# Kernel optimization log

Hardware: AMD Instinct MI355X
Metric: run time of the kernel (lower is better)

Reference implementation:

```python
import jax, jax.numpy as jnp
import numpy as np

B, S, E, HD = 32, 1024, 768, 64
NUM_IMAGE_PATCHES = 49


def setup_inputs() -> dict:
    key = jax.random.key(0)
    ks = jax.random.split(key, 9)
    w = 0.02
    return {
        "decoder_sequence": jax.random.normal(ks[0], (B, S, E), dtype=jnp.float32),
        "Wq": jax.random.normal(ks[1], (E, HD), dtype=jnp.float32) * w,
        "bq": jnp.zeros((HD,), dtype=jnp.float32),
        "Wk": jax.random.normal(ks[2], (E, HD), dtype=jnp.float32) * w,
        "bk": jnp.zeros((HD,), dtype=jnp.float32),
        "Wv": jax.random.normal(ks[3], (E, HD), dtype=jnp.float32) * w,
        "bv": jnp.zeros((HD,), dtype=jnp.float32),
        "input_sequence_length": 975,
        "padding_mask": jax.random.randint(ks[4], (B, 1, S), 0, 2).astype(bool),
    }


def reference(decoder_sequence, Wq, bq, Wk, bk, Wv, bv, input_sequence_length, padding_mask):
    # single-head projections: [B,S,E] @ [E,HD] -> [B,S,HD]
    Q = decoder_sequence @ Wq + bq
    K = decoder_sequence @ Wk + bk
    V = decoder_sequence @ Wv + bv

    scores = jnp.einsum('bid,bjd->bij', Q, K) / jnp.sqrt(jnp.float32(HD))

    # mask: image-patch rows (i < 49) fully unmasked; text region is causal
    # (mask[49:,49:] = triu(-inf, diag=1)), i.e. -inf where i >= 49 and j > i.
    i = jnp.arange(S)[:, None]
    j = jnp.arange(S)[None, :]
    causal_bad = (i >= NUM_IMAGE_PATCHES) & (j > i)  # [S,S]
    scores = jnp.where(causal_bad[None, :, :], -jnp.inf, scores)

    # padding mask on keys, broadcast over queries: [B,1,S] -> [B,S,S]
    scores = jnp.where(padding_mask, -jnp.inf, scores)

    A = jax.nn.softmax(scores, axis=-1)
    H = jnp.einsum('bij,bjd->bid', A, V)
    return H
```

## Files before the change

### kernel.cpp

```cpp
#include <hip/hip_runtime.h>
#include <stdint.h>
#include <stddef.h>


typedef __attribute__((ext_vector_type(8))) short bf16x8;
typedef __attribute__((ext_vector_type(4))) float f32x4;

#define NIP 49
#define QSCALE 0.18033688011112042f

__device__ __forceinline__ short f2b(float f) {
  union { float f; uint32_t u; } c; c.f = f;
  uint32_t u = c.u;
  uint32_t r = (u + 0x7fffu + ((u >> 16) & 1u)) >> 16;
  return (short)(uint16_t)r;
}

__global__ __launch_bounds__(256) void wt_kernel(
    const float* __restrict__ Wq, const float* __restrict__ Wk,
    const float* __restrict__ Wv, short* __restrict__ Wt) {
  int idx = blockIdx.x * 256 + threadIdx.x;
  int n = idx % 192;
  int k = idx / 192;
  const float* W = (n < 64) ? Wq : (n < 128) ? Wk : Wv;
  int h = n & 63;
  Wt[(size_t)n * 768 + k] = f2b(W[(size_t)k * 64 + h]);
}

__global__ __launch_bounds__(256) void proj_kernel(
    const float* __restrict__ X, const float* __restrict__ bq,
    const float* __restrict__ bk, const float* __restrict__ bv,
    const short* __restrict__ Wt, short* __restrict__ Qg,
    short* __restrict__ Kg, short* __restrict__ Vg) {
  __shared__ short lX[64][40];
  __shared__ short lW[192][40];
  const int tid = threadIdx.x;
  const int wid = tid >> 6;
  const int lane = tid & 63;
  const int l15 = lane & 15;
  const int q4 = lane >> 4;
  const int r0 = blockIdx.x * 64;

  f32x4 acc[12];
#pragma unroll
  for (int c = 0; c < 12; ++c) acc[c] = (f32x4){0.f, 0.f, 0.f, 0.f};

  for (int k0 = 0; k0 < 768; k0 += 32) {
    __syncthreads();
#pragma unroll
    for (int i = 0; i < 2; ++i) {
      int idx = tid + i * 256;
      int row = idx >> 3, c4 = idx & 7;
      float4 v = *(const float4*)(X + (size_t)(r0 + row) * 768 + k0 + c4 * 4);
      short4 sv;
      sv.x = f2b(v.x); sv.y = f2b(v.y); sv.z = f2b(v.z); sv.w = f2b(v.w);
      *(short4*)&lX[row][c4 * 4] = sv;
    }
#pragma unroll
    for (int i = 0; i < 3; ++i) {
      int idx = tid + i * 256;
      int row = idx >> 2, seg = idx & 3;
      *(int4*)&lW[row][seg * 8] = *(const int4*)(Wt + (size_t)row * 768 + k0 + seg * 8);
    }
    __syncthreads();
    bf16x8 a = *(const bf16x8*)&lX[wid * 16 + l15][q4 * 8];
#pragma unroll
    for (int c = 0; c < 12; ++c) {
      bf16x8 bw = *(const bf16x8*)&lW[c * 16 + l15][q4 * 8];
      acc[c] = __builtin_amdgcn_mfma_f32_16x16x32_bf16(a, bw, acc[c], 0, 0, 0);
    }
  }
#pragma unroll
  for (int c = 0; c < 12; ++c) {
    const int mtx = c >> 2;
    const int h = (c & 3) * 16 + l15;
    const float* bp = (mtx == 0) ? bq : (mtx == 1) ? bk : bv;
    short* op = (mtx == 0) ? Qg : (mtx == 1) ? Kg : Vg;
    const float bias = bp[h];
#pragma unroll
    for (int rr = 0; rr < 4; ++rr) {
      int row = r0 + wid * 16 + q4 * 4 + rr;
      float v = acc[c][rr] + bias;
      if (mtx == 0) v *= QSCALE;
      op[(size_t)row * 64 + h] = f2b(v);
    }
  }
}

__global__ __launch_bounds__(256) void attn_kernel(
    const short* __restrict__ Qg, const short* __restrict__ Kg,
    const short* __restrict__ Vg, const int* __restrict__ pad,
    float* __restrict__ out) {
  __shared__ short lK[64][72];
  __shared__ short lV[64][72];
  __shared__ short lP[4][16][72];
  __shared__ float lpad[64];

  const int t = blockIdx.x, b = blockIdx.y;
  const int tid = threadIdx.x;
  const int wid = tid >> 6;
  const int lane = tid & 63;
  const int l15 = lane & 15;
  const int q4 = lane >> 4;
  const int qs = t * 64;
  const size_t base = (size_t)b * 1024;

  short(*lQ)[72] = (short(*)[72])lP;
#pragma unroll
  for (int i = 0; i < 2; ++i) {
    int idx = tid + i * 256;
    int row = idx >> 3, seg = idx & 7;
    *(int4*)&lQ[row][seg * 8] = *(const int4*)(Qg + (base + qs + row) * 64 + seg * 8);
  }
  __syncthreads();
  bf16x8 aq0 = *(const bf16x8*)&lQ[wid * 16 + l15][q4 * 8];
  bf16x8 aq1 = *(const bf16x8*)&lQ[wid * 16 + l15][32 + q4 * 8];

  f32x4 o[4];
  float m_run[4], l_run[4];
#pragma unroll
  for (int c = 0; c < 4; ++c) o[c] = (f32x4){0.f, 0.f, 0.f, 0.f};
#pragma unroll
  for (int rr = 0; rr < 4; ++rr) { m_run[rr] = -1e30f; l_run[rr] = 0.f; }

  const int nkt = (t == 0) ? 16 : (t + 1);
  for (int kt = 0; kt < nkt; ++kt) {
    const int kb = kt * 64;
    __syncthreads();
#pragma unroll
    for (int i = 0; i < 2; ++i) {
      int idx = tid + i * 256;
      int row = idx >> 3, seg = idx & 7;
      *(int4*)&lK[row][seg * 8] = *(const int4*)(Kg + (base + kb + row) * 64 + seg * 8);
    }
#pragma unroll
    for (int i = 0; i < 2; ++i) {
      int idx = tid + i * 256;
      int row = idx >> 3, seg = idx & 7;
      short tmp[8];
      *(int4*)tmp = *(const int4*)(Vg + (base + kb + row) * 64 + seg * 8);
#pragma unroll
      for (int j = 0; j < 8; ++j) lV[seg * 8 + j][row] = tmp[j];
    }
    if (tid < 64) lpad[tid] = (pad[base + kb + tid] != 0) ? -1e30f : 0.0f;
    __syncthreads();

    f32x4 s[4];
#pragma unroll
    for (int c = 0; c < 4; ++c) {
      s[c] = (f32x4){0.f, 0.f, 0.f, 0.f};
      bf16x8 b0 = *(const bf16x8*)&lK[c * 16 + l15][q4 * 8];
      s[c] = __builtin_amdgcn_mfma_f32_16x16x32_bf16(aq0, b0, s[c], 0, 0, 0);
      bf16x8 b1 = *(const bf16x8*)&lK[c * 16 + l15][32 + q4 * 8];
      s[c] = __builtin_amdgcn_mfma_f32_16x16x32_bf16(aq1, b1, s[c], 0, 0, 0);
    }

    float padv[4];
#pragma unroll
    for (int c = 0; c < 4; ++c) padv[c] = lpad[c * 16 + l15];

    float p[4][4];
#pragma unroll
    for (int rr = 0; rr < 4; ++rr) {
      const int qi = qs + wid * 16 + q4 * 4 + rr;
      float zmax = -1e30f;
#pragma unroll
      for (int c = 0; c < 4; ++c) {
        float z = s[c][rr] + padv[c];
        int j = kb + c * 16 + l15;
        if (qi >= NIP && j > qi) z = -1e30f;
        p[c][rr] = z;
        zmax = fmaxf(zmax, z);
      }
#pragma unroll
      for (int off = 1; off < 16; off <<= 1)
        zmax = fmaxf(zmax, __shfl_xor(zmax, off, 64));
      const float mn = fmaxf(m_run[rr], zmax);
      const float alpha = exp2f(m_run[rr] - mn);
      m_run[rr] = mn;
      float rs = 0.f;
#pragma unroll
      for (int c = 0; c < 4; ++c) {
        float pv = exp2f(p[c][rr] - mn);
        p[c][rr] = pv;
        rs += pv;
      }
#pragma unroll
      for (int off = 1; off < 16; off <<= 1)
        rs += __shfl_xor(rs, off, 64);
      l_run[rr] = l_run[rr] * alpha + rs;
#pragma unroll
      for (int c = 0; c < 4; ++c) o[c][rr] *= alpha;
    }

#pragma unroll
    for (int rr = 0; rr < 4; ++rr)
#pragma unroll
      for (int c = 0; c < 4; ++c)
        lP[wid][q4 * 4 + rr][c * 16 + l15] = f2b(p[c][rr]);
    __syncthreads();

    bf16x8 ap0 = *(const bf16x8*)&lP[wid][l15][q4 * 8];
    bf16x8 ap1 = *(const bf16x8*)&lP[wid][l15][32 + q4 * 8];
#pragma unroll
    for (int c = 0; c < 4; ++c) {
      bf16x8 bv0 = *(const bf16x8*)&lV[c * 16 + l15][q4 * 8];
      o[c] = __builtin_amdgcn_mfma_f32_16x16x32_bf16(ap0, bv0, o[c], 0, 0, 0);
      bf16x8 bv1 = *(const bf16x8*)&lV[c * 16 + l15][32 + q4 * 8];
      o[c] = __builtin_amdgcn_mfma_f32_16x16x32_bf16(ap1, bv1, o[c], 0, 0, 0);
    }
  }

#pragma unroll
  for (int rr = 0; rr < 4; ++rr) {
    const float inv = (l_run[rr] > 0.f) ? 1.0f / l_run[rr] : 0.f;
    const size_t row = base + qs + wid * 16 + q4 * 4 + rr;
#pragma unroll
    for (int c = 0; c < 4; ++c)
      out[row * 64 + c * 16 + l15] = o[c][rr] * inv;
  }
}

extern "C" void kernel_launch(void* const* d_in, const int* in_sizes, int n_in,
                              void* d_out, int out_size, void* d_ws, size_t ws_size,
                              hipStream_t stream) {
  const float* X  = (const float*)d_in[0];
  const float* Wq = (const float*)d_in[1];
  const float* bq = (const float*)d_in[2];
  const float* Wk = (const float*)d_in[3];
  const float* bk = (const float*)d_in[4];
  const float* Wv = (const float*)d_in[5];
  const float* bv = (const float*)d_in[6];
  const int* pad  = (const int*)d_in[8];
  float* out = (float*)d_out;

  short* Qg = (short*)d_ws;
  short* Kg = Qg + 32768 * 64;
  short* Vg = Kg + 32768 * 64;
  short* Wt = Vg + 32768 * 64;

  wt_kernel<<<576, 256, 0, stream>>>(Wq, Wk, Wv, Wt);
  proj_kernel<<<512, 256, 0, stream>>>(X, bq, bk, bv, Wt, Qg, Kg, Vg);
  attn_kernel<<<dim3(16, 32), 256, 0, stream>>>(Qg, Kg, Vg, pad, out);
}
```

Baseline: 237.9 us.

## Double-buffer projection and attention tiles, store V transposed, reorder causal tiles

Measured after the change: 217.8 us. -8.4%, faster.

```diff
diff --git a/kernel.cpp b/kernel.cpp
--- a/kernel.cpp
+++ b/kernel.cpp
@@ -8,6 +8,7 @@
 
 #define NIP 49
 #define QSCALE 0.18033688011112042f
+#define SOFT_BARRIER() asm volatile("s_waitcnt lgkmcnt(0)\n\ts_barrier" ::: "memory")
 
 __device__ __forceinline__ short f2b(float f) {
   union { float f; uint32_t u; } c; c.f = f;
@@ -20,83 +21,107 @@
     const float* __restrict__ Wq, const float* __restrict__ Wk,
     const float* __restrict__ Wv, short* __restrict__ Wt) {
   int idx = blockIdx.x * 256 + threadIdx.x;
-  int n = idx % 192;
-  int k = idx / 192;
+  int n = idx / 768;
+  int k = idx - n * 768;
   const float* W = (n < 64) ? Wq : (n < 128) ? Wk : Wv;
-  int h = n & 63;
-  Wt[(size_t)n * 768 + k] = f2b(W[(size_t)k * 64 + h]);
-}
-
-__global__ __launch_bounds__(256) void proj_kernel(
+  Wt[idx] = f2b(W[(size_t)k * 64 + (n & 63)]);
+}
+
+__global__ __launch_bounds__(512, 4) void proj_kernel(
     const float* __restrict__ X, const float* __restrict__ bq,
     const float* __restrict__ bk, const float* __restrict__ bv,
     const short* __restrict__ Wt, short* __restrict__ Qg,
-    short* __restrict__ Kg, short* __restrict__ Vg) {
-  __shared__ short lX[64][40];
-  __shared__ short lW[192][40];
+    short* __restrict__ Kg, short* __restrict__ Vt) {
+  __shared__ short lX[2][64][40];
+  __shared__ short lW[2][192][40];
   const int tid = threadIdx.x;
   const int wid = tid >> 6;
   const int lane = tid & 63;
   const int l15 = lane & 15;
   const int q4 = lane >> 4;
+  const int mw = wid & 3;
+  const int nh = wid >> 2;
   const int r0 = blockIdx.x * 64;
 
-  f32x4 acc[12];
-#pragma unroll
-  for (int c = 0; c < 12; ++c) acc[c] = (f32x4){0.f, 0.f, 0.f, 0.f};
-
-  for (int k0 = 0; k0 < 768; k0 += 32) {
-    __syncthreads();
-#pragma unroll
-    for (int i = 0; i < 2; ++i) {
-      int idx = tid + i * 256;
-      int row = idx >> 3, c4 = idx & 7;
-      float4 v = *(const float4*)(X + (size_t)(r0 + row) * 768 + k0 + c4 * 4);
+  const int xrow = tid >> 3, xc4 = tid & 7;
+  const int wrow0 = tid >> 2, wseg0 = tid & 3;
+  const int wrow1 = (tid + 512) >> 2, wseg1 = tid & 3;
+
+  float4 rx;
+  int4 rw0, rw1;
+  auto loadg = [&](int k0) {
+    rx = *(const float4*)(X + (size_t)(r0 + xrow) * 768 + k0 + xc4 * 4);
+    rw0 = *(const int4*)(Wt + (size_t)wrow0 * 768 + k0 + wseg0 * 8);
+    if (tid < 256)
+      rw1 = *(const int4*)(Wt + (size_t)wrow1 * 768 + k0 + wseg1 * 8);
+  };
+  auto stage = [&](int buf) {
+    short4 sv;
+    sv.x = f2b(rx.x); sv.y = f2b(rx.y); sv.z = f2b(rx.z); sv.w = f2b(rx.w);
+    *(short4*)&lX[buf][xrow][xc4 * 4] = sv;
+    *(int4*)&lW[buf][wrow0][wseg0 * 8] = rw0;
+    if (tid < 256) *(int4*)&lW[buf][wrow1][wseg1 * 8] = rw1;
+  };
+
+  f32x4 acc[6];
+#pragma unroll
+  for (int c = 0; c < 6; ++c) acc[c] = (f32x4){0.f, 0.f, 0.f, 0.f};
+
+  loadg(0);
+  stage(0);
+  loadg(32);
+  SOFT_BARRIER();
+  for (int st = 0; st < 24; ++st) {
+    const int cur = st & 1;
+    bf16x8 a = *(const bf16x8*)&lX[cur][mw * 16 + l15][q4 * 8];
+#pragma unroll
+    for (int c = 0; c < 6; ++c) {
+      bf16x8 bw = *(const bf16x8*)&lW[cur][(nh * 6 + c) * 16 + l15][q4 * 8];
+      acc[c] = __builtin_amdgcn_mfma_f32_16x16x32_bf16(a, bw, acc[c], 0, 0, 0);
+    }
+    if (st + 1 < 24) {
+      stage(cur ^ 1);
+      if (st + 2 < 24) loadg((st + 2) * 32);
+    }
+    SOFT_BARRIER();
+  }
+  const int b = r0 >> 10, s0 = r0 & 1023;
+#pragma unroll
+  for (int c = 0; c < 6; ++c) {
+    const int ct = nh * 6 + c;
+    const int mtx = ct >> 2;
+    const int h = (ct & 3) * 16 + l15;
+    if (mtx < 2) {
+      const float bias = (mtx == 0 ? bq : bk)[h];
+      short* op = (mtx == 0) ? Qg : Kg;
+#pragma unroll
+      for (int rr = 0; rr < 4; ++rr) {
+        int row = r0 + mw * 16 + q4 * 4 + rr;
+        float v = acc[c][rr] + bias;
+        if (mtx == 0) v *= QSCALE;
+        op[(size_t)row * 64 + h] = f2b(v);
+      }
+    } else {
+      const float bias = bv[h];
       short4 sv;
-      sv.x = f2b(v.x); sv.y = f2b(v.y); sv.z = f2b(v.z); sv.w = f2b(v.w);
-      *(short4*)&lX[row][c4 * 4] = sv;
-    }
-#pragma unroll
-    for (int i = 0; i < 3; ++i) {
-      int idx = tid + i * 256;
-      int row = idx >> 2, seg = idx & 3;
-      *(int4*)&lW[row][seg * 8] = *(const int4*)(Wt + (size_t)row * 768 + k0 + seg * 8);
-    }
-    __syncthreads();
-    bf16x8 a = *(const bf16x8*)&lX[wid * 16 + l15][q4 * 8];
-#pragma unroll
-    for (int c = 0; c < 12; ++c) {
-      bf16x8 bw = *(const bf16x8*)&lW[c * 16 + l15][q4 * 8];
-      acc[c] = __builtin_amdgcn_mfma_f32_16x16x32_bf16(a, bw, acc[c], 0, 0, 0);
-    }
-  }
-#pragma unroll
-  for (int c = 0; c < 12; ++c) {
-    const int mtx = c >> 2;
-    const int h = (c & 3) * 16 + l15;
-    const float* bp = (mtx == 0) ? bq : (mtx == 1) ? bk : bv;
-    short* op = (mtx == 0) ? Qg : (mtx == 1) ? Kg : Vg;
-    const float bias = bp[h];
-#pragma unroll
-    for (int rr = 0; rr < 4; ++rr) {
-      int row = r0 + wid * 16 + q4 * 4 + rr;
-      float v = acc[c][rr] + bias;
-      if (mtx == 0) v *= QSCALE;
-      op[(size_t)row * 64 + h] = f2b(v);
-    }
-  }
-}
-
-__global__ __launch_bounds__(256) void attn_kernel(
+      sv.x = f2b(acc[c][0] + bias); sv.y = f2b(acc[c][1] + bias);
+      sv.z = f2b(acc[c][2] + bias); sv.w = f2b(acc[c][3] + bias);
+      *(short4*)(Vt + ((size_t)(b * 64 + h) << 10) + s0 + mw * 16 + q4 * 4) = sv;
+    }
+  }
+}
+
+__global__ __launch_bounds__(256, 3) void attn_kernel(
     const short* __restrict__ Qg, const short* __restrict__ Kg,
-    const short* __restrict__ Vg, const int* __restrict__ pad,
+    const short* __restrict__ Vt, const int* __restrict__ pad,
     float* __restrict__ out) {
-  __shared__ short lK[64][72];
-  __shared__ short lV[64][72];
+  __shared__ short lK[2][64][72];
+  __shared__ short lV[2][64][72];
   __shared__ short lP[4][16][72];
-  __shared__ float lpad[64];
-
-  const int t = blockIdx.x, b = blockIdx.y;
+  __shared__ float lpad[2][64];
+
+  const int bx = blockIdx.x, b = blockIdx.y;
+  const int t = (bx == 0) ? 0 : 16 - bx;
   const int tid = threadIdx.x;
   const int wid = tid >> 6;
   const int lane = tid & 63;
@@ -104,15 +129,40 @@
   const int q4 = lane >> 4;
   const int qs = t * 64;
   const size_t base = (size_t)b * 1024;
+  const int nkt = (t == 0) ? 16 : (t + 1);
 
   short(*lQ)[72] = (short(*)[72])lP;
-#pragma unroll
-  for (int i = 0; i < 2; ++i) {
-    int idx = tid + i * 256;
-    int row = idx >> 3, seg = idx & 7;
+  {
+    int row = tid >> 3, seg = tid & 7;
     *(int4*)&lQ[row][seg * 8] = *(const int4*)(Qg + (base + qs + row) * 64 + seg * 8);
-  }
-  __syncthreads();
+    row = (tid + 256) >> 3;
+    *(int4*)&lQ[row][seg * 8] = *(const int4*)(Qg + (base + qs + row) * 64 + seg * 8);
+  }
+
+  const int srow = tid >> 3, sseg = tid & 7;
+  int4 rk0, rk1, rv0, rv1;
+  float rpad;
+  auto loadg = [&](int kt) {
+    const int kb = kt * 64;
+    rk0 = *(const int4*)(Kg + (base + kb + srow) * 64 + sseg * 8);
+    rk1 = *(const int4*)(Kg + (base + kb + srow + 32) * 64 + sseg * 8);
+    rv0 = *(const int4*)(Vt + ((size_t)(b * 64 + srow) << 10) + kb + sseg * 8);
+    rv1 = *(const int4*)(Vt + ((size_t)(b * 64 + srow + 32) << 10) + kb + sseg * 8);
+    rpad = (tid < 64) ? ((pad[base + kb + tid] != 0) ? -1e30f : 0.0f) : 0.0f;
+  };
+  auto stage = [&](int buf) {
+    *(int4*)&lK[buf][srow][sseg * 8] = rk0;
+    *(int4*)&lK[buf][srow + 32][sseg * 8] = rk1;
+    *(int4*)&lV[buf][srow][sseg * 8] = rv0;
+    *(int4*)&lV[buf][srow + 32][sseg * 8] = rv1;
+    if (tid < 64) lpad[buf][tid] = rpad;
+  };
+
+  loadg(0);
+  stage(0);
+  if (nkt > 1) loadg(1);
+  SOFT_BARRIER();
+
   bf16x8 aq0 = *(const bf16x8*)&lQ[wid * 16 + l15][q4 * 8];
   bf16x8 aq1 = *(const bf16x8*)&lQ[wid * 16 + l15][32 + q4 * 8];
 
@@ -123,41 +173,23 @@
 #pragma unroll
   for (int rr = 0; rr < 4; ++rr) { m_run[rr] = -1e30f; l_run[rr] = 0.f; }
 
-  const int nkt = (t == 0) ? 16 : (t + 1);
   for (int kt = 0; kt < nkt; ++kt) {
+    const int cur = kt & 1;
     const int kb = kt * 64;
-    __syncthreads();
-#pragma unroll
-    for (int i = 0; i < 2; ++i) {
-      int idx = tid + i * 256;
-      int row = idx >> 3, seg = idx & 7;
-      *(int4*)&lK[row][seg * 8] = *(const int4*)(Kg + (base + kb + row) * 64 + seg * 8);
-    }
-#pragma unroll
-    for (int i = 0; i < 2; ++i) {
-      int idx = tid + i * 256;
-      int row = idx >> 3, seg = idx & 7;
-      short tmp[8];
-      *(int4*)tmp = *(const int4*)(Vg + (base + kb + row) * 64 + seg * 8);
-#pragma unroll
-      for (int j = 0; j < 8; ++j) lV[seg * 8 + j][row] = tmp[j];
-    }
-    if (tid < 64) lpad[tid] = (pad[base + kb + tid] != 0) ? -1e30f : 0.0f;
-    __syncthreads();
-
-    f32x4 s[4];
+    const bool causal = (t == 0) || (kt == t);
+
+    f32x4 s4[4];
 #pragma unroll
     for (int c = 0; c < 4; ++c) {
-      s[c] = (f32x4){0.f, 0.f, 0.f, 0.f};
-      bf16x8 b0 = *(const bf16x8*)&lK[c * 16 + l15][q4 * 8];
-      s[c] = __builtin_amdgcn_mfma_f32_16x16x32_bf16(aq0, b0, s[c], 0, 0, 0);
-      bf16x8 b1 = *(const bf16x8*)&lK[c * 16 + l15][32 + q4 * 8];
-      s[c] = __builtin_amdgcn_mfma_f32_16x16x32_bf16(aq1, b1, s[c], 0, 0, 0);
-    }
-
+      s4[c] = (f32x4){0.f, 0.f, 0.f, 0.f};
+      bf16x8 b0 = *(const bf16x8*)&lK[cur][c * 16 + l15][q4 * 8];
+      s4[c] = __builtin_amdgcn_mfma_f32_16x16x32_bf16(aq0, b0, s4[c], 0, 0, 0);
+      bf16x8 b1 = *(const bf16x8*)&lK[cur][c * 16 + l15][32 + q4 * 8];
+      s4[c] = __builtin_amdgcn_mfma_f32_16x16x32_bf16(aq1, b1, s4[c], 0, 0, 0);
+    }
     float padv[4];
 #pragma unroll
-    for (int c = 0; c < 4; ++c) padv[c] = lpad[c * 16 + l15];
+    for (int c = 0; c < 4; ++c) padv[c] = lpad[cur][c * 16 + l15];
 
     float p[4][4];
 #pragma unroll
@@ -166,9 +198,11 @@
       float zmax = -1e30f;
 #pragma unroll
       for (int c = 0; c < 4; ++c) {
-        float z = s[c][rr] + padv[c];
-        int j = kb + c * 16 + l15;
-        if (qi >= NIP && j > qi) z = -1e30f;
+        float z = s4[c][rr] + padv[c];
+        if (causal) {
+          int j = kb + c * 16 + l15;
+          if (qi >= NIP && j > qi) z = -1e30f;
+        }
         p[c][rr] = z;
         zmax = fmaxf(zmax, z);
       }
@@ -198,17 +232,22 @@
 #pragma unroll
       for (int c = 0; c < 4; ++c)
         lP[wid][q4 * 4 + rr][c * 16 + l15] = f2b(p[c][rr]);
-    __syncthreads();
 
     bf16x8 ap0 = *(const bf16x8*)&lP[wid][l15][q4 * 8];
     bf16x8 ap1 = *(const bf16x8*)&lP[wid][l15][32 + q4 * 8];
 #pragma unroll
     for (int c = 0; c < 4; ++c) {
-      bf16x8 bv0 = *(const bf16x8*)&lV[c * 16 + l15][q4 * 8];
+      bf16x8 bv0 = *(const bf16x8*)&lV[cur][c * 16 + l15][q4 * 8];
       o[c] = __builtin_amdgcn_mfma_f32_16x16x32_bf16(ap0, bv0, o[c], 0, 0, 0);
-      bf16x8 bv1 = *(const bf16x8*)&lV[c * 16 + l15][32 + q4 * 8];
+      bf16x8 bv1 = *(const bf16x8*)&lV[cur][c * 16 + l15][32 + q4 * 8];
       o[c] = __builtin_amdgcn_mfma_f32_16x16x32_bf16(ap1, bv1, o[c], 0, 0, 0);
     }
+
+    if (kt + 1 < nkt) {
+      stage(cur ^ 1);
+      if (kt + 2 < nkt) loadg(kt + 2);
+    }
+    SOFT_BARRIER();
   }
 
 #pragma unroll
@@ -236,10 +275,10 @@
 
   short* Qg = (short*)d_ws;
   short* Kg = Qg + 32768 * 64;
-  short* Vg = Kg + 32768 * 64;
-  short* Wt = Vg + 32768 * 64;
+  short* Vt = Kg + 32768 * 64;
+  short* Wt = Vt + 32768 * 64;
 
   wt_kernel<<<576, 256, 0, stream>>>(Wq, Wk, Wv, Wt);
-  proj_kernel<<<512, 256, 0, stream>>>(X, bq, bk, bv, Wt, Qg, Kg, Vg);
-  attn_kernel<<<dim3(16, 32), 256, 0, stream>>>(Qg, Kg, Vg, pad, out);
-}
+  proj_kernel<<<512, 512, 0, stream>>>(X, bq, bk, bv, Wt, Qg, Kg, Vt);
+  attn_kernel<<<dim3(16, 32), 256, 0, stream>>>(Qg, Kg, Vt, pad, out);
+}
```
